# Performance work log

Measured on AMD Instinct MI355X. Metric: run time of the kernel, lower is better.

## Reference

```python
import jax, jax.numpy as jnp
import numpy as np

B, S, E = 4, 2048, 1024
H = 16
D = E // H  # head_dim = 64


def setup_inputs() -> dict:
    key = jax.random.key(0)
    k1, k2, k3 = jax.random.split(key, 3)
    x = jax.random.normal(k1, (B, S, E), dtype=jnp.float32)
    w_qkv = jax.random.normal(k2, (E, 3 * E), dtype=jnp.float32) * (E ** -0.5)
    b_qkv = jnp.zeros((3 * E,), dtype=jnp.float32)
    w_proj = jax.random.normal(k3, (E, E), dtype=jnp.float32) * (E ** -0.5)
    b_proj = jnp.zeros((E,), dtype=jnp.float32)
    return {"x": x, "w_qkv": w_qkv, "b_qkv": b_qkv, "w_proj": w_proj, "b_proj": b_proj}


def reference(x, w_qkv, b_qkv, w_proj, b_proj):
    bsz, seq_len, emb = x.shape
    scale = D ** -0.5
    qkv = x @ w_qkv + b_qkv                      # [B,S,3E]
    q, k, v = jnp.split(qkv, 3, axis=2)
    # [B,S,E] -> [B,H,S,D]
    q = q.reshape(bsz, seq_len, H, D).transpose(0, 2, 1, 3)
    k = k.reshape(bsz, seq_len, H, D).transpose(0, 2, 1, 3)
    v = v.reshape(bsz, seq_len, H, D).transpose(0, 2, 1, 3)
    att = jnp.einsum('bhqd,bhkd->bhqk', q, k) * scale
    causal = jnp.tril(jnp.ones((seq_len, seq_len), dtype=bool))
    att = jnp.where(causal, att, -jnp.inf)
    att = jax.nn.softmax(att, axis=-1)
    y = jnp.einsum('bhqk,bhkd->bhqd', att, v)
    y = y.transpose(0, 2, 1, 3).reshape(bsz, seq_len, emb)
    return y @ w_proj + b_proj
```

## Files before the change

kernel.cpp:

```cpp
#include <hip/hip_runtime.h>
#include <hip/hip_bf16.h>
#include <stdint.h>

#define S_LEN 2048
#define EMB   1024
#define NH    16
#define HD    64

typedef unsigned short u16;
typedef __attribute__((ext_vector_type(2))) float f32x2;
typedef __attribute__((ext_vector_type(4))) float f32x4;
typedef __attribute__((ext_vector_type(8))) short bf16x8;

typedef __attribute__((address_space(1))) const unsigned char gas_t;
typedef __attribute__((address_space(3))) unsigned char las_t;

static __device__ __forceinline__ void gld_lds16(const void* g, void* l) {
  __builtin_amdgcn_global_load_lds((gas_t*)g, (las_t*)l, 16, 0, 0);
}

static __device__ __forceinline__ u16 f2bf(float f) {
  unsigned int u = __builtin_bit_cast(unsigned int, f);
  u = u + 0x7fffu + ((u >> 16) & 1u);
  return (u16)(u >> 16);
}

static __device__ __forceinline__ float fexp2(float x) {
  float r;
  asm("v_exp_f32 %0, %1" : "=v"(r) : "v"(x));
  return r;
}

static __device__ __forceinline__ unsigned cvt_pk_bf16(float lo, float hi) {
  unsigned r;
  asm("v_cvt_pk_bf16_f32 %0, %1, %2" : "=v"(r) : "v"(lo), "v"(hi));
  return r;
}

static __device__ __forceinline__ f32x2 pk_add(f32x2 a, f32x2 b) {
  f32x2 r;
  asm("v_pk_add_f32 %0, %1, %2" : "=v"(r) : "v"(a), "v"(b));
  return r;
}

static __device__ __forceinline__ float red4rows_max(float x) {
  unsigned u = __builtin_bit_cast(unsigned, x);
  auto r = __builtin_amdgcn_permlane32_swap(u, u, false, false);
  float y = fmaxf(__builtin_bit_cast(float, (unsigned)r[0]),
                  __builtin_bit_cast(float, (unsigned)r[1]));
  unsigned v = __builtin_bit_cast(unsigned, y);
  auto r2 = __builtin_amdgcn_permlane16_swap(v, v, false, false);
  return fmaxf(__builtin_bit_cast(float, (unsigned)r2[0]),
               __builtin_bit_cast(float, (unsigned)r2[1]));
}
static __device__ __forceinline__ float red4rows_sum(float x) {
  unsigned u = __builtin_bit_cast(unsigned, x);
  auto r = __builtin_amdgcn_permlane32_swap(u, u, false, false);
  float y = __builtin_bit_cast(float, (unsigned)r[0]) +
            __builtin_bit_cast(float, (unsigned)r[1]);
  unsigned v = __builtin_bit_cast(unsigned, y);
  auto r2 = __builtin_amdgcn_permlane16_swap(v, v, false, false);
  return __builtin_bit_cast(float, (unsigned)r2[0]) +
         __builtin_bit_cast(float, (unsigned)r2[1]);
}

__global__ __launch_bounds__(256) void k_prep(const float* __restrict__ x,
                                              u16* __restrict__ xb,
                                              const float* __restrict__ w_qkv,
                                              u16* __restrict__ wqkvT,
                                              const float* __restrict__ w_proj,
                                              u16* __restrict__ wprojT) {
  __shared__ u16 tile[64][68];
  const int bid = blockIdx.x;
  const int t = threadIdx.x;
  if (bid < 1024) {
    const int n4 = (8192 * 1024) / 4;
    int i = bid * 256 + t;
    for (; i < n4; i += 1024 * 256) {
      float4 f = ((const float4*)x)[i];
      ushort4 o;
      o.x = f2bf(f.x); o.y = f2bf(f.y); o.z = f2bf(f.z); o.w = f2bf(f.w);
      ((ushort4*)xb)[i] = o;
    }
    return;
  }
  const float* W;
  u16* WT;
  int c0, r0, K, N;
  if (bid < 1792) {
    const int idx = bid - 1024;
    W = w_qkv; WT = wqkvT; K = 1024; N = 3072;
    c0 = (idx % 48) * 64; r0 = (idx / 48) * 64;
  } else {
    const int idx = bid - 1792;
    W = w_proj; WT = wprojT; K = 1024; N = 1024;
    c0 = (idx & 15) * 64; r0 = (idx >> 4) * 64;
  }
  const int tr = t >> 4, tc4 = (t & 15) * 4;
#pragma unroll
  for (int i = 0; i < 4; i++) {
    const int r = tr + 16 * i;
    float4 f = *(const float4*)&W[(size_t)(r0 + r) * N + c0 + tc4];
    ushort4 o;
    o.x = f2bf(f.x); o.y = f2bf(f.y); o.z = f2bf(f.z); o.w = f2bf(f.w);
    *(ushort4*)&tile[r][tc4] = o;
  }
  __syncthreads();
  const int oc = t >> 2, or0 = (t & 3) * 16;
  u16 vals[16];
#pragma unroll
  for (int j = 0; j < 16; j++) vals[j] = tile[or0 + j][oc];
  u16* dst = &WT[(size_t)(c0 + oc) * K + r0 + or0];
  *(uint4*)dst = *(const uint4*)&vals[0];
  *(uint4*)(dst + 8) = *(const uint4*)&vals[8];
}

template <int MODE>
__global__ __launch_bounds__(256) void k_gemm(const u16* __restrict__ A,
                                              const u16* __restrict__ BT,
                                              const float* __restrict__ bias,
                                              float* __restrict__ Cout,
                                              u16* __restrict__ q_ws,
                                              u16* __restrict__ k_ws,
                                              u16* __restrict__ v_t,
                                              int N, int K) {
  __shared__ u16 As[2][128 * 32];
  __shared__ u16 Bs[2][128 * 32];
  const int tid = threadIdx.x;
  const int w = tid >> 6, lane = tid & 63;
  const int wr = w >> 1, wc = w & 1;
  const int lrow = lane & 15, lk8 = (lane >> 4) * 8;
  const int orig = blockIdx.y * gridDim.x + blockIdx.x;
  const int total = gridDim.x * gridDim.y;
  const int wgid = (orig & 7) * (total >> 3) + (orig >> 3);
  const int bxn = wgid % gridDim.x;
  const int byn = wgid / gridDim.x;
  const int brow = byn * 128, bcol = bxn * 128;
  const int srow = lane >> 2;
  const int scol = (lane & 3) * 8;

  const f32x4 zero = {0.f, 0.f, 0.f, 0.f};
  f32x4 acc[4][4];
#pragma unroll
  for (int m = 0; m < 4; m++)
#pragma unroll
    for (int n = 0; n < 4; n++) acc[m][n] = zero;

  auto stage = [&](int kt, int buf) {
#pragma unroll
    for (int i = 0; i < 2; i++) {
      const int c = w * 2 + i;
      const int row = c * 16 + srow;
      gld_lds16(&A[(size_t)(brow + row) * K + kt + scol], (void*)(&As[buf][c * 512]));
      gld_lds16(&BT[(size_t)(bcol + row) * K + kt + scol], (void*)(&Bs[buf][c * 512]));
    }
  };

  const int NK = K >> 5;
  stage(0, 0);
  __syncthreads();
  for (int it = 0; it < NK; ++it) {
    const int cur = it & 1;
    if (it + 1 < NK) stage((it + 1) << 5, cur ^ 1);
    bf16x8 af[4], bfr[4];
#pragma unroll
    for (int mt = 0; mt < 4; mt++)
      af[mt] = *(const bf16x8*)&As[cur][(wr * 64 + mt * 16 + lrow) * 32 + lk8];
#pragma unroll
    for (int nt = 0; nt < 4; nt++)
      bfr[nt] = *(const bf16x8*)&Bs[cur][(wc * 64 + nt * 16 + lrow) * 32 + lk8];
    __builtin_amdgcn_s_setprio(1);
#pragma unroll
    for (int mt = 0; mt < 4; mt++)
#pragma unroll
      for (int nt = 0; nt < 4; nt++)
        acc[mt][nt] = __builtin_amdgcn_mfma_f32_16x16x32_bf16(af[mt], bfr[nt],
                                                              acc[mt][nt], 0, 0, 0);
    __builtin_amdgcn_s_setprio(0);
    __syncthreads();
  }

  if constexpr (MODE == 0) {
    const int which = bcol >> 10;
#pragma unroll
    for (int mt = 0; mt < 4; mt++)
#pragma unroll
      for (int nt = 0; nt < 4; nt++) {
        const int col = bcol + wc * 64 + nt * 16 + lrow;
        const int e = col & 1023;
        const int h = e >> 6, d = e & 63;
        const int row0 = brow + wr * 64 + mt * 16 + (lane >> 4) * 4;
        const int b = row0 >> 11, s0 = row0 & 2047;
        const size_t bh = (size_t)(b * NH + h);
        const float bv = bias[col];
        if (which == 2) {
          ushort4 pk;
          pk.x = f2bf(acc[mt][nt][0] + bv);
          pk.y = f2bf(acc[mt][nt][1] + bv);
          pk.z = f2bf(acc[mt][nt][2] + bv);
          pk.w = f2bf(acc[mt][nt][3] + bv);
          *(ushort4*)&v_t[(bh * HD + d) * S_LEN + s0] = pk;
        } else {
          u16* dst = which ? k_ws : q_ws;
#pragma unroll
          for (int r = 0; r < 4; r++)
            dst[(bh * S_LEN + s0 + r) * HD + d] = f2bf(acc[mt][nt][r] + bv);
        }
      }
  } else {
#pragma unroll
    for (int mt = 0; mt < 4; mt++)
#pragma unroll
      for (int nt = 0; nt < 4; nt++)
#pragma unroll
        for (int r = 0; r < 4; r++) {
          const int row = brow + wr * 64 + mt * 16 + (lane >> 4) * 4 + r;
          const int col = bcol + wc * 64 + nt * 16 + lrow;
          Cout[(size_t)row * N + col] = acc[mt][nt][r] + bias[col];
        }
  }
}

__global__ __launch_bounds__(256, 2) void k_attn(const u16* __restrict__ q_ws,
                                                 const u16* __restrict__ k_ws,
                                                 const u16* __restrict__ v_t,
                                                 u16* __restrict__ y) {
  __shared__ u16 Kl[2][64 * 64];
  __shared__ u16 Vl[2][64 * 64];
  const int tid = threadIdx.x;
  const int w = tid >> 6, lane = tid & 63;
  const int lrow = lane & 15, lk8 = (lane >> 4) * 8;
  const int g4 = (lane >> 4) * 4;
  const int f = blockIdx.y * 16 + blockIdx.x;
  const int pr = (f >> 3) & 15;
  const int bh = (f & 7) + ((f >> 7) << 3);
  const int tileA = pr, tileB = 31 - pr;
  const size_t base = (size_t)bh * S_LEN * HD;
  const float SC = 0.125f * 1.4426950408889634f;

  bf16x8 qfA[2], qfB[2];
#pragma unroll
  for (int ks = 0; ks < 2; ks++) {
    qfA[ks] = *(const bf16x8*)&q_ws[base + (size_t)(tileA * 64 + w * 16 + lrow) * HD + ks * 32 + lk8];
    qfB[ks] = *(const bf16x8*)&q_ws[base + (size_t)(tileB * 64 + w * 16 + lrow) * HD + ks * 32 + lk8];
  }

  const f32x4 zero = {0.f, 0.f, 0.f, 0.f};
  f32x4 oA[4], oB[4];
#pragma unroll
  for (int dt = 0; dt < 4; dt++) { oA[dt] = zero; oB[dt] = zero; }
  float mA = -1e30f, lA = 0.f, mB = -1e30f, lB = 0.f;

  auto stage = [&](int jb, int buf) {
#pragma unroll
    for (int i = 0; i < 2; i++) {
      const int c = w * 2 + i;
      const int row = c * 8 + (lane >> 3);
      const int blk = (lane & 7) ^ (row & 7);
      gld_lds16(&k_ws[base + (size_t)(jb * 64 + row) * HD + blk * 8],
                (void*)(&Kl[buf][c * 512]));
      gld_lds16(&v_t[base + (size_t)row * S_LEN + jb * 64 + blk * 8],
                (void*)(&Vl[buf][c * 512]));
    }
  };

  auto qk = [&](const bf16x8 (&kf)[2][4], const bf16x8 (&qf)[2], f32x4 (&sa)[4]) {
#pragma unroll
    for (int nt = 0; nt < 4; nt++) sa[nt] = zero;
#pragma unroll
    for (int ks = 0; ks < 2; ks++)
#pragma unroll
      for (int nt = 0; nt < 4; nt++)
        sa[nt] = __builtin_amdgcn_mfma_f32_16x16x32_bf16(kf[ks][nt], qf[ks], sa[nt], 0, 0, 0);
  };

  auto softmax = [&](f32x4 (&sa)[4], f32x4 (&o)[4], float& m_run, float& l_run,
                     bool maskDiag, bf16x8 (&pfrag)[2]) {
    float sv[4][4];
    if (maskDiag) {
#pragma unroll
      for (int nt = 0; nt < 4; nt++)
#pragma unroll
        for (int r = 0; r < 4; r++)
          sv[nt][r] = ((nt * 16 + g4 + r) > (w * 16 + lrow)) ? -3.0e38f : sa[nt][r];
    } else {
#pragma unroll
      for (int nt = 0; nt < 4; nt++)
#pragma unroll
        for (int r = 0; r < 4; r++) sv[nt][r] = sa[nt][r];
    }

    float mx = fmaxf(fmaxf(fmaxf(sv[0][0], sv[0][1]), fmaxf(sv[0][2], sv[0][3])),
                     fmaxf(fmaxf(sv[1][0], sv[1][1]), fmaxf(sv[1][2], sv[1][3])));
    mx = fmaxf(mx,
               fmaxf(fmaxf(fmaxf(sv[2][0], sv[2][1]), fmaxf(sv[2][2], sv[2][3])),
                     fmaxf(fmaxf(sv[3][0], sv[3][1]), fmaxf(sv[3][2], sv[3][3]))));
    mx = red4rows_max(mx);
    const float mxs = mx * SC;
    const bool nogrow = __all(mxs <= m_run + 8.0f);
    float mn = m_run;
    if (!nogrow) {
      mn = fmaxf(m_run, mxs);
      const float alpha = fexp2(m_run - mn);
      l_run *= alpha;
#pragma unroll
      for (int dt = 0; dt < 4; dt++) o[dt] *= alpha;
      m_run = mn;
    }
    const float nmn = -mn;
    f32x2 p2[4][2];
#pragma unroll
    for (int nt = 0; nt < 4; nt++)
#pragma unroll
      for (int h = 0; h < 2; h++) {
        const float a = fexp2(__builtin_fmaf(sv[nt][2 * h], SC, nmn));
        const float b = fexp2(__builtin_fmaf(sv[nt][2 * h + 1], SC, nmn));
        f32x2 p; p[0] = a; p[1] = b;
        p2[nt][h] = p;
      }
    f32x2 s0 = pk_add(p2[0][0], p2[0][1]);
    f32x2 s1 = pk_add(p2[1][0], p2[1][1]);
    f32x2 s2 = pk_add(p2[2][0], p2[2][1]);
    f32x2 s3 = pk_add(p2[3][0], p2[3][1]);
    s0 = pk_add(s0, s1);
    s2 = pk_add(s2, s3);
    s0 = pk_add(s0, s2);
    float sum = s0[0] + s0[1];
    sum = red4rows_sum(sum);
    l_run += sum;

    unsigned pk[4][2];
#pragma unroll
    for (int nt = 0; nt < 4; nt++) {
      pk[nt][0] = cvt_pk_bf16(p2[nt][0][0], p2[nt][0][1]);
      pk[nt][1] = cvt_pk_bf16(p2[nt][1][0], p2[nt][1][1]);
    }
    union { unsigned u[4]; bf16x8 v; } c0, c1;
    {
      auto r0 = __builtin_amdgcn_permlane32_swap(pk[0][0], pk[1][0], false, false);
      auto s0p = __builtin_amdgcn_permlane16_swap(r0[0], r0[1], false, false);
      auto r1 = __builtin_amdgcn_permlane32_swap(pk[0][1], pk[1][1], false, false);
      auto s1p = __builtin_amdgcn_permlane16_swap(r1[0], r1[1], false, false);
      c0.u[0] = s0p[0]; c0.u[1] = s1p[0]; c0.u[2] = s0p[1]; c0.u[3] = s1p[1];
      auto r2 = __builtin_amdgcn_permlane32_swap(pk[2][0], pk[3][0], false, false);
      auto s2p = __builtin_amdgcn_permlane16_swap(r2[0], r2[1], false, false);
      auto r3 = __builtin_amdgcn_permlane32_swap(pk[2][1], pk[3][1], false, false);
      auto s3p = __builtin_amdgcn_permlane16_swap(r3[0], r3[1], false, false);
      c1.u[0] = s2p[0]; c1.u[1] = s3p[0]; c1.u[2] = s2p[1]; c1.u[3] = s3p[1];
    }
    pfrag[0] = c0.v;
    pfrag[1] = c1.v;
  };

  stage(0, 0);
  __syncthreads();
  for (int jb = 0; jb <= tileB; jb++) {
    const int cur = jb & 1;
    if (jb < tileB) stage(jb + 1, cur ^ 1);
    const bool doA = (jb <= tileA);

    bf16x8 kf[2][4];
#pragma unroll
    for (int ks = 0; ks < 2; ks++)
#pragma unroll
      for (int nt = 0; nt < 4; nt++) {
        const int kvr = nt * 16 + lrow;
        const int blk = (ks * 4 + (lane >> 4)) ^ (kvr & 7);
        kf[ks][nt] = *(const bf16x8*)&Kl[cur][kvr * 64 + blk * 8];
      }
    f32x4 saB[4], saA[4];
    __builtin_amdgcn_s_setprio(1);
    qk(kf, qfB, saB);
    if (doA) qk(kf, qfA, saA);
    __builtin_amdgcn_s_setprio(0);

    bf16x8 pfB[2], pfA[2];
    softmax(saB, oB, mB, lB, jb == tileB, pfB);
    if (doA) softmax(saA, oA, mA, lA, jb == tileA, pfA);

    bf16x8 vf[2][4];
#pragma unroll
    for (int ks = 0; ks < 2; ks++)
#pragma unroll
      for (int dt = 0; dt < 4; dt++) {
        const int vr = dt * 16 + lrow;
        const int vblk = (ks * 4 + (lane >> 4)) ^ (vr & 7);
        vf[ks][dt] = *(const bf16x8*)&Vl[cur][vr * 64 + vblk * 8];
      }

    __builtin_amdgcn_s_setprio(1);
#pragma unroll
    for (int ks = 0; ks < 2; ks++)
#pragma unroll
      for (int dt = 0; dt < 4; dt++)
        oB[dt] = __builtin_amdgcn_mfma_f32_16x16x32_bf16(vf[ks][dt], pfB[ks], oB[dt], 0, 0, 0);
    if (doA) {
#pragma unroll
      for (int ks = 0; ks < 2; ks++)
#pragma unroll
        for (int dt = 0; dt < 4; dt++)
          oA[dt] = __builtin_amdgcn_mfma_f32_16x16x32_bf16(vf[ks][dt], pfA[ks], oA[dt], 0, 0, 0);
    }
    __builtin_amdgcn_s_setprio(0);
    __syncthreads();
  }

  const int b = bh >> 4, h = bh & 15;
  const float invA = 1.0f / lA;
  const float invB = 1.0f / lB;
  const int qgA = tileA * 64 + w * 16 + lrow;
  const int qgB = tileB * 64 + w * 16 + lrow;
#pragma unroll
  for (int dt = 0; dt < 4; dt++) {
    uint2 pa, pb;
    pa.x = cvt_pk_bf16(oA[dt][0] * invA, oA[dt][1] * invA);
    pa.y = cvt_pk_bf16(oA[dt][2] * invA, oA[dt][3] * invA);
    pb.x = cvt_pk_bf16(oB[dt][0] * invB, oB[dt][1] * invB);
    pb.y = cvt_pk_bf16(oB[dt][2] * invB, oB[dt][3] * invB);
    *(uint2*)&y[(size_t)(b * S_LEN + qgA) * EMB + h * HD + dt * 16 + g4] = pa;
    *(uint2*)&y[(size_t)(b * S_LEN + qgB) * EMB + h * HD + dt * 16 + g4] = pb;
  }
}

extern "C" void kernel_launch(void* const* d_in, const int* in_sizes, int n_in,
                              void* d_out, int out_size, void* d_ws, size_t ws_size,
                              hipStream_t stream) {
  const float* x      = (const float*)d_in[0];
  const float* w_qkv  = (const float*)d_in[1];
  const float* b_qkv  = (const float*)d_in[2];
  const float* w_proj = (const float*)d_in[3];
  const float* b_proj = (const float*)d_in[4];
  float* out = (float*)d_out;

  char* ws = (char*)d_ws;
  u16* wqkvT  = (u16*)(ws);
  u16* wprojT = (u16*)(ws + 6291456);
  u16* xb     = (u16*)(ws + 8388608);
  u16* q_ws   = (u16*)(ws + 25165824);
  u16* k_ws   = (u16*)(ws + 41943040);
  u16* v_t    = (u16*)(ws + 58720256);
  u16* y_att  = xb;

  k_prep<<<dim3(2048), dim3(256), 0, stream>>>(x, xb, w_qkv, wqkvT, w_proj, wprojT);
  k_gemm<0><<<dim3(24, 64), dim3(256), 0, stream>>>(xb, wqkvT, b_qkv, nullptr,
                                                    q_ws, k_ws, v_t, 3072, 1024);
  k_attn<<<dim3(16, 64), dim3(256), 0, stream>>>(q_ws, k_ws, v_t, y_att);
  k_gemm<1><<<dim3(8, 64), dim3(256), 0, stream>>>(y_att, wprojT, b_proj, out,
                                                   nullptr, nullptr, nullptr, 1024, 1024);
}
```

Baseline: 184.6 us.

## Load K/V fragments directly from global memory, dropping LDS staging and barriers

The attention kernel no longer stages K and V tiles into double-buffered shared memory through global_load_lds. Each wave now reads its MFMA fragments straight from global memory, with V loads issued before the softmax to hide their latency. This removes the LDS footprint and the per-iteration __syncthreads. In exchange, all four waves read the same K/V data redundantly from global memory or cache, and the prefetch pipelining across iterations is lost.

```diff
diff --git a/kernel.cpp b/kernel.cpp
--- a/kernel.cpp
+++ b/kernel.cpp
@@ -225,8 +225,6 @@
                                                  const u16* __restrict__ k_ws,
                                                  const u16* __restrict__ v_t,
                                                  u16* __restrict__ y) {
-  __shared__ u16 Kl[2][64 * 64];
-  __shared__ u16 Vl[2][64 * 64];
   const int tid = threadIdx.x;
   const int w = tid >> 6, lane = tid & 63;
   const int lrow = lane & 15, lk8 = (lane >> 4) * 8;
@@ -250,19 +248,6 @@
 #pragma unroll
   for (int dt = 0; dt < 4; dt++) { oA[dt] = zero; oB[dt] = zero; }
   float mA = -1e30f, lA = 0.f, mB = -1e30f, lB = 0.f;
-
-  auto stage = [&](int jb, int buf) {
-#pragma unroll
-    for (int i = 0; i < 2; i++) {
-      const int c = w * 2 + i;
-      const int row = c * 8 + (lane >> 3);
-      const int blk = (lane & 7) ^ (row & 7);
-      gld_lds16(&k_ws[base + (size_t)(jb * 64 + row) * HD + blk * 8],
-                (void*)(&Kl[buf][c * 512]));
-      gld_lds16(&v_t[base + (size_t)row * S_LEN + jb * 64 + blk * 8],
-                (void*)(&Vl[buf][c * 512]));
-    }
-  };
 
   auto qk = [&](const bf16x8 (&kf)[2][4], const bf16x8 (&qf)[2], f32x4 (&sa)[4]) {
 #pragma unroll
@@ -352,42 +337,35 @@
     pfrag[1] = c1.v;
   };
 
-  stage(0, 0);
-  __syncthreads();
   for (int jb = 0; jb <= tileB; jb++) {
-    const int cur = jb & 1;
-    if (jb < tileB) stage(jb + 1, cur ^ 1);
     const bool doA = (jb <= tileA);
 
+    const u16* kp = k_ws + base + ((size_t)(jb * 64) + lrow) * HD + lk8;
     bf16x8 kf[2][4];
 #pragma unroll
     for (int ks = 0; ks < 2; ks++)
 #pragma unroll
-      for (int nt = 0; nt < 4; nt++) {
-        const int kvr = nt * 16 + lrow;
-        const int blk = (ks * 4 + (lane >> 4)) ^ (kvr & 7);
-        kf[ks][nt] = *(const bf16x8*)&Kl[cur][kvr * 64 + blk * 8];
-      }
+      for (int nt = 0; nt < 4; nt++)
+        kf[ks][nt] = *(const bf16x8*)&kp[nt * (16 * HD) + ks * 32];
+
     f32x4 saB[4], saA[4];
     __builtin_amdgcn_s_setprio(1);
     qk(kf, qfB, saB);
     if (doA) qk(kf, qfA, saA);
     __builtin_amdgcn_s_setprio(0);
 
+    const u16* vp = v_t + base + (size_t)lrow * S_LEN + jb * 64 + lk8;
+    bf16x8 vf[2][4];
+#pragma unroll
+    for (int ks = 0; ks < 2; ks++)
+#pragma unroll
+      for (int dt = 0; dt < 4; dt++)
+        vf[ks][dt] = *(const bf16x8*)&vp[(size_t)dt * (16 * S_LEN) + ks * 32];
+
     bf16x8 pfB[2], pfA[2];
     softmax(saB, oB, mB, lB, jb == tileB, pfB);
     if (doA) softmax(saA, oA, mA, lA, jb == tileA, pfA);
 
-    bf16x8 vf[2][4];
-#pragma unroll
-    for (int ks = 0; ks < 2; ks++)
-#pragma unroll
-      for (int dt = 0; dt < 4; dt++) {
-        const int vr = dt * 16 + lrow;
-        const int vblk = (ks * 4 + (lane >> 4)) ^ (vr & 7);
-        vf[ks][dt] = *(const bf16x8*)&Vl[cur][vr * 64 + vblk * 8];
-      }
-
     __builtin_amdgcn_s_setprio(1);
 #pragma unroll
     for (int ks = 0; ks < 2; ks++)
@@ -402,7 +380,6 @@
           oA[dt] = __builtin_amdgcn_mfma_f32_16x16x32_bf16(vf[ks][dt], pfA[ks], oA[dt], 0, 0, 0);
     }
     __builtin_amdgcn_s_setprio(0);
-    __syncthreads();
   }
 
   const int b = bh >> 4, h = bh & 15;
```

Result: slower. 344.7 us (+86.7%).
